# Kernel tuning notes

Hardware: AMD Instinct MI355X
Metric: run time of the kernel (lower is better)

The kernel has to match this reference:

```python
import jax, jax.numpy as jnp
import numpy as np

NPOINT = 1024   # npoint
K = 20          # num_samples[0]


def _fps(pts, npoint):
    """Iterative furthest point sampling. pts: [N,3] -> indices [npoint] (starts at idx 0)."""
    N = pts.shape[0]

    def step(carry, _):
        min_d, last = carry
        d = jnp.sum((pts - pts[last]) ** 2, axis=-1)          # [N] dist to last selected
        min_d = jnp.minimum(min_d, d)                          # running min-dist to selected set
        nxt = jnp.argmax(min_d).astype(jnp.int32)
        return (min_d, nxt), nxt

    init = (jnp.full((N,), 1e10, pts.dtype), jnp.int32(0))
    _, rest = jax.lax.scan(step, init, None, length=npoint - 1)
    return jnp.concatenate([jnp.zeros((1,), jnp.int32), rest])


def _pdist2(q, p):
    """Squared pairwise distances. q:[M,3], p:[N,3] -> [M,N], clamped to >=0 (matches pdist2squared)."""
    d = jnp.sum(q * q, -1)[:, None] + jnp.sum(p * p, -1)[None, :] - 2.0 * (q @ p.T)
    return jnp.maximum(d, 0.0)


def _knn(q, p, k):
    """k nearest neighbors of each q among p, dropping the closest (self), ascending order."""
    d = _pdist2(q, p)                       # [M,N]
    _, idx = jax.lax.top_k(-d, k + 1)       # ascending distance order
    return idx[:, 1:]                       # drop self, [M,k]


def setup_inputs() -> dict:
    key = jax.random.key(0)
    points = jax.random.normal(key, (4, 16384, 3), dtype=jnp.float32)
    return {"points": points}


def reference(points):
    B, N, _ = points.shape
    # --- FPS node sampling (Sample module) ---
    xyz_ind = jax.vmap(lambda p: _fps(p, NPOINT))(points)                  # [B, N1]
    xyz_query = jnp.take_along_axis(points, xyz_ind[:, :, None], axis=1)  # [B, N1, 3]

    # --- Gmid: neighbors of the N1 query points among all N points ---
    nbr_mid = jax.vmap(lambda q, p: _knn(q, p, K))(xyz_query, points)      # [B, N1, K]
    src_mid = jnp.take_along_axis(points, nbr_mid.reshape(B, -1, 1), axis=1).reshape(B, NPOINT, K, 3)
    d_mid = xyz_query[:, :, None, :] - src_mid                             # edata['d'] = pos[dst]-pos[src]

    # --- Gout: neighbors among the downsampled N1 points themselves ---
    nbr_out = jax.vmap(lambda q: _knn(q, q, K))(xyz_query)                 # [B, N1, K]
    src_out = jnp.take_along_axis(xyz_query, nbr_out.reshape(B, -1, 1), axis=1).reshape(B, NPOINT, K, 3)
    d_out = xyz_query[:, :, None, :] - src_out

    return xyz_ind, xyz_query, nbr_mid, d_mid, nbr_out, d_out
```

## Files before the change

kernel.cpp:

```cpp
#include <hip/hip_runtime.h>
#include <stdint.h>

#define BATCH   4
#define NPTS    16384
#define NPOINT  1024
#define KNN     20
#define KSEL    21

#define FPS_THREADS 512
#define PPT (NPTS / FPS_THREADS)

__global__ __launch_bounds__(FPS_THREADS)
void fps_kernel(const float* __restrict__ pts, float* __restrict__ out,
                int* __restrict__ ws_ind, float* __restrict__ ws_query) {
  const int b = blockIdx.x;
  const float* P = pts + (size_t)b * NPTS * 3;
  float* out_ind = out;
  float* out_q   = out + BATCH * NPOINT;
  const int t = threadIdx.x;

  float px[PPT], py[PPT], pz[PPT], md[PPT];
#pragma unroll
  for (int i = 0; i < PPT; ++i) {
    int idx = i * FPS_THREADS + t;
    px[i] = P[idx * 3 + 0];
    py[i] = P[idx * 3 + 1];
    pz[i] = P[idx * 3 + 2];
    md[i] = 1e10f;
  }

  __shared__ float s_val[FPS_THREADS / 64];
  __shared__ int   s_idx[FPS_THREADS / 64];

  if (t == 0) {
    out_ind[b * NPOINT] = 0.0f;
    ws_ind[b * NPOINT]  = 0;
    float ax = P[0], ay = P[1], az = P[2];
    out_q[(size_t)(b * NPOINT) * 3 + 0] = ax;
    out_q[(size_t)(b * NPOINT) * 3 + 1] = ay;
    out_q[(size_t)(b * NPOINT) * 3 + 2] = az;
    ws_query[(size_t)(b * NPOINT) * 3 + 0] = ax;
    ws_query[(size_t)(b * NPOINT) * 3 + 1] = ay;
    ws_query[(size_t)(b * NPOINT) * 3 + 2] = az;
  }
  float qx = P[0], qy = P[1], qz = P[2];

  for (int it = 1; it < NPOINT; ++it) {
    float best = -1.0f;
    int bi = 0;
#pragma unroll
    for (int i = 0; i < PPT; ++i) {
      float dx = __fsub_rn(px[i], qx);
      float dy = __fsub_rn(py[i], qy);
      float dz = __fsub_rn(pz[i], qz);
      float d  = __fadd_rn(__fadd_rn(__fmul_rn(dx, dx), __fmul_rn(dy, dy)),
                           __fmul_rn(dz, dz));
      float m = fminf(md[i], d);
      md[i] = m;
      if (m > best) { best = m; bi = i; }
    }
    int bidx = bi * FPS_THREADS + t;

#pragma unroll
    for (int off = 32; off >= 1; off >>= 1) {
      float ov = __shfl_down(best, off);
      int   oi = __shfl_down(bidx, off);
      if (ov > best || (ov == best && oi < bidx)) { best = ov; bidx = oi; }
    }

    __syncthreads();
    if ((t & 63) == 0) { s_val[t >> 6] = best; s_idx[t >> 6] = bidx; }
    __syncthreads();

    float bv = s_val[0];
    int   bx = s_idx[0];
#pragma unroll
    for (int w = 1; w < FPS_THREADS / 64; ++w) {
      float v = s_val[w];
      int   x = s_idx[w];
      if (v > bv || (v == bv && x < bx)) { bv = v; bx = x; }
    }

    qx = P[bx * 3 + 0];
    qy = P[bx * 3 + 1];
    qz = P[bx * 3 + 2];

    if (t == 0) {
      out_ind[b * NPOINT + it] = (float)bx;
      ws_ind[b * NPOINT + it]  = bx;
      size_t o = (size_t)(b * NPOINT + it) * 3;
      out_q[o + 0] = qx; out_q[o + 1] = qy; out_q[o + 2] = qz;
      ws_query[o + 0] = qx; ws_query[o + 1] = qy; ws_query[o + 2] = qz;
    }
  }
}

#define KNN_WAVES 4

__global__ __launch_bounds__(256)
void knn_kernel(const float* __restrict__ cand_base,
                const float* __restrict__ query_base,
                int ncand,
                float* __restrict__ out_nbr,
                float* __restrict__ out_d) {
#pragma clang fp contract(off)
  const int wid_in_blk = threadIdx.x >> 6;
  const int w    = blockIdx.x * KNN_WAVES + wid_in_blk;
  const int lane = threadIdx.x & 63;
  const int b    = w / NPOINT;
  const int qi   = w % NPOINT;

  const float* C = cand_base + (size_t)b * ncand * 3;
  const float* Q = query_base + ((size_t)b * NPOINT + qi) * 3;
  const float qx = Q[0], qy = Q[1], qz = Q[2];
  const float qq = (qx * qx + qy * qy) + qz * qz;

  unsigned long long best[KSEL];
#pragma unroll
  for (int j = 0; j < KSEL; ++j) best[j] = 0xFFFFFFFFFFFFFFFFull;

  for (int j = lane; j < ncand; j += 64) {
    float px = C[j * 3 + 0], py = C[j * 3 + 1], pz = C[j * 3 + 2];
    float pp  = (px * px + py * py) + pz * pz;
    float dot = __builtin_fmaf(qz, pz, __builtin_fmaf(qy, py, qx * px));
    float d = (qq + pp) - 2.0f * dot;
    d = fmaxf(d, 0.0f);
    unsigned long long key =
        ((unsigned long long)__float_as_uint(d) << 32) | (unsigned int)j;
    if (key < best[KSEL - 1]) {
      unsigned long long c = key;
#pragma unroll
      for (int s = 0; s < KSEL; ++s) {
        unsigned long long o = best[s];
        bool l = c < o;
        unsigned long long nb = l ? c : o;
        c = l ? o : c;
        best[s] = nb;
      }
    }
  }

  __shared__ unsigned long long s_list[KNN_WAVES][64 * KSEL];
  unsigned long long* L = s_list[wid_in_blk];
#pragma unroll
  for (int j = 0; j < KSEL; ++j) L[lane * KSEL + j] = best[j];
  __syncthreads();

  int hp = 0;
  int myK = -1, myIdx = 0;
  for (int r = 0; r < KSEL; ++r) {
    unsigned long long v = L[lane * KSEL + hp];
    int src = lane;
#pragma unroll
    for (int off = 32; off >= 1; off >>= 1) {
      unsigned long long ov = __shfl_down(v, off);
      int os = __shfl_down(src, off);
      if (ov < v) { v = ov; src = os; }
    }
    v   = __shfl(v, 0);
    src = __shfl(src, 0);
    if (lane == src) hp++;
    if (r >= 1 && lane == r - 1) {
      myIdx = (int)(unsigned int)(v & 0xFFFFFFFFull);
      myK = r - 1;
    }
  }

  if (myK >= 0) {
    size_t o = (size_t)(b * NPOINT + qi) * KNN + myK;
    out_nbr[o] = (float)myIdx;
    float sx = C[myIdx * 3 + 0], sy = C[myIdx * 3 + 1], sz = C[myIdx * 3 + 2];
    out_d[o * 3 + 0] = qx - sx;
    out_d[o * 3 + 1] = qy - sy;
    out_d[o * 3 + 2] = qz - sz;
  }
}

extern "C" void kernel_launch(void* const* d_in, const int* in_sizes, int n_in,
                              void* d_out, int out_size, void* d_ws,
                              size_t ws_size, hipStream_t stream) {
  (void)in_sizes; (void)n_in; (void)out_size; (void)ws_size;
  const float* pts = (const float*)d_in[0];
  float* out = (float*)d_out;

  int*   ws_ind   = (int*)d_ws;
  float* ws_query = (float*)((char*)d_ws + (size_t)BATCH * NPOINT * sizeof(int));

  float* out_nbr_mid = out + (size_t)BATCH * NPOINT * 4;
  float* out_d_mid   = out_nbr_mid + (size_t)BATCH * NPOINT * KNN;
  float* out_nbr_out = out_d_mid + (size_t)BATCH * NPOINT * KNN * 3;
  float* out_d_out   = out_nbr_out + (size_t)BATCH * NPOINT * KNN;

  hipLaunchKernelGGL(fps_kernel, dim3(BATCH), dim3(FPS_THREADS), 0, stream,
                     pts, out, ws_ind, ws_query);

  hipLaunchKernelGGL(knn_kernel, dim3(BATCH * NPOINT / KNN_WAVES), dim3(256),
                     0, stream, pts, ws_query, NPTS, out_nbr_mid, out_d_mid);

  hipLaunchKernelGGL(knn_kernel, dim3(BATCH * NPOINT / KNN_WAVES), dim3(256),
                     0, stream, ws_query, ws_query, NPOINT, out_nbr_out,
                     out_d_out);
}
```

Measured before the change: 2.868 ms.

## Split FPS across 16 cooperating blocks per batch with global atomic slot exchange

FPS now runs on 16 blocks per batch instead of one, each holding 4 points per thread, and reduces the per-iteration argmax across blocks through release/acquire atomic stores into an iteration-tagged slot array in the workspace. This spreads the serial sampling loop over many more CUs so each iteration does less per-thread work. In exchange every iteration pays a cross-block spin-wait through L2/global memory. The scheme also assumes all 64 blocks are co-resident, and it relies on the slot memory not already holding a matching iteration tag from an earlier run.

Measured after the change: 3.038 ms. 5.9% more time.

```diff
diff --git a/kernel.cpp b/kernel.cpp
--- a/kernel.cpp
+++ b/kernel.cpp
@@ -7,59 +7,71 @@
 #define KNN     20
 #define KSEL    21
 
-#define FPS_THREADS 512
-#define PPT (NPTS / FPS_THREADS)
-
-__global__ __launch_bounds__(FPS_THREADS)
+typedef unsigned long long u64;
+
+#define FPS_SUBS 16
+#define FPS_TPB  256
+#define FPS_GT   (FPS_SUBS * FPS_TPB)
+#define FPS_PPT  (NPTS / FPS_GT)
+
+#define REPEAT4(M) M(0) M(1) M(2) M(3)
+
+#define FPS_DECL(i) float px##i, py##i, pz##i, md##i;
+
+#define FPS_INIT(i) { \
+    int idx = (i) * FPS_GT + g; \
+    px##i = P[idx * 3 + 0]; \
+    py##i = P[idx * 3 + 1]; \
+    pz##i = P[idx * 3 + 2]; \
+    md##i = 1e10f; }
+
+#define FPS_STEP(i) { \
+    float dx = __fsub_rn(px##i, qx); \
+    float dy = __fsub_rn(py##i, qy); \
+    float dz = __fsub_rn(pz##i, qz); \
+    float d  = __fadd_rn(__fadd_rn(__fmul_rn(dx, dx), __fmul_rn(dy, dy)), \
+                         __fmul_rn(dz, dz)); \
+    float m = fminf(md##i, d); \
+    md##i = m; \
+    bool g2 = (m > best); \
+    best = g2 ? m : best; \
+    bi   = g2 ? (i) : bi; }
+
+__global__ __launch_bounds__(FPS_TPB)
 void fps_kernel(const float* __restrict__ pts, float* __restrict__ out,
-                int* __restrict__ ws_ind, float* __restrict__ ws_query) {
-  const int b = blockIdx.x;
+                int* __restrict__ ws_ind, float* __restrict__ ws_query,
+                u64* __restrict__ slots) {
+  const int blk = blockIdx.x;
+  const int b   = blk >> 4;
+  const int sub = blk & 15;
+  const int t   = threadIdx.x;
+  const int g   = sub * FPS_TPB + t;
   const float* P = pts + (size_t)b * NPTS * 3;
   float* out_ind = out;
   float* out_q   = out + BATCH * NPOINT;
-  const int t = threadIdx.x;
-
-  float px[PPT], py[PPT], pz[PPT], md[PPT];
-#pragma unroll
-  for (int i = 0; i < PPT; ++i) {
-    int idx = i * FPS_THREADS + t;
-    px[i] = P[idx * 3 + 0];
-    py[i] = P[idx * 3 + 1];
-    pz[i] = P[idx * 3 + 2];
-    md[i] = 1e10f;
-  }
-
-  __shared__ float s_val[FPS_THREADS / 64];
-  __shared__ int   s_idx[FPS_THREADS / 64];
-
-  if (t == 0) {
+
+  REPEAT4(FPS_DECL)
+  REPEAT4(FPS_INIT)
+
+  __shared__ float s_val[FPS_TPB / 64];
+  __shared__ int   s_idx[FPS_TPB / 64];
+  __shared__ int   s_widx;
+
+  if (sub == 0 && t == 0) {
     out_ind[b * NPOINT] = 0.0f;
     ws_ind[b * NPOINT]  = 0;
     float ax = P[0], ay = P[1], az = P[2];
-    out_q[(size_t)(b * NPOINT) * 3 + 0] = ax;
-    out_q[(size_t)(b * NPOINT) * 3 + 1] = ay;
-    out_q[(size_t)(b * NPOINT) * 3 + 2] = az;
-    ws_query[(size_t)(b * NPOINT) * 3 + 0] = ax;
-    ws_query[(size_t)(b * NPOINT) * 3 + 1] = ay;
-    ws_query[(size_t)(b * NPOINT) * 3 + 2] = az;
+    size_t o0 = (size_t)(b * NPOINT) * 3;
+    out_q[o0 + 0] = ax; out_q[o0 + 1] = ay; out_q[o0 + 2] = az;
+    ws_query[o0 + 0] = ax; ws_query[o0 + 1] = ay; ws_query[o0 + 2] = az;
   }
   float qx = P[0], qy = P[1], qz = P[2];
 
   for (int it = 1; it < NPOINT; ++it) {
     float best = -1.0f;
     int bi = 0;
-#pragma unroll
-    for (int i = 0; i < PPT; ++i) {
-      float dx = __fsub_rn(px[i], qx);
-      float dy = __fsub_rn(py[i], qy);
-      float dz = __fsub_rn(pz[i], qz);
-      float d  = __fadd_rn(__fadd_rn(__fmul_rn(dx, dx), __fmul_rn(dy, dy)),
-                           __fmul_rn(dz, dz));
-      float m = fminf(md[i], d);
-      md[i] = m;
-      if (m > best) { best = m; bi = i; }
-    }
-    int bidx = bi * FPS_THREADS + t;
+    REPEAT4(FPS_STEP)
+    int bidx = bi * FPS_GT + g;
 
 #pragma unroll
     for (int off = 32; off >= 1; off >>= 1) {
@@ -67,27 +79,52 @@
       int   oi = __shfl_down(bidx, off);
       if (ov > best || (ov == best && oi < bidx)) { best = ov; bidx = oi; }
     }
-
-    __syncthreads();
     if ((t & 63) == 0) { s_val[t >> 6] = best; s_idx[t >> 6] = bidx; }
     __syncthreads();
 
-    float bv = s_val[0];
-    int   bx = s_idx[0];
-#pragma unroll
-    for (int w = 1; w < FPS_THREADS / 64; ++w) {
-      float v = s_val[w];
-      int   x = s_idx[w];
-      if (v > bv || (v == bv && x < bx)) { bv = v; bx = x; }
-    }
-
-    qx = P[bx * 3 + 0];
-    qy = P[bx * 3 + 1];
-    qz = P[bx * 3 + 2];
-
-    if (t == 0) {
-      out_ind[b * NPOINT + it] = (float)bx;
-      ws_ind[b * NPOINT + it]  = bx;
+    if (t < 64) {
+      float bv = s_val[0];
+      int   bx = s_idx[0];
+#pragma unroll
+      for (int w = 1; w < FPS_TPB / 64; ++w) {
+        float v = s_val[w];
+        int   x = s_idx[w];
+        if (v > bv || (v == bv && x < bx)) { bv = v; bx = x; }
+      }
+      u64* row = slots + (size_t)it * (BATCH * FPS_SUBS) + b * FPS_SUBS;
+      if (t == 0) {
+        u64 pv = ((u64)__float_as_uint(bv) << 32) |
+                 (unsigned)(bx | (it << 20));
+        __hip_atomic_store(&row[sub], pv, __ATOMIC_RELEASE,
+                           __HIP_MEMORY_SCOPE_AGENT);
+      }
+      int j = t & 15;
+      u64 v;
+      do {
+        v = __hip_atomic_load(&row[j], __ATOMIC_ACQUIRE,
+                              __HIP_MEMORY_SCOPE_AGENT);
+      } while ((v >> 63) != 0 ||
+               (((unsigned)(v >> 20)) & 0x3FFu) != (unsigned)it);
+      float fv = __uint_as_float((unsigned)(v >> 32));
+      int   fi = (int)((unsigned)v & 0xFFFFFu);
+#pragma unroll
+      for (int off = 8; off >= 1; off >>= 1) {
+        float ofv = __shfl_down(fv, off);
+        int   ofi = __shfl_down(fi, off);
+        if (ofv > fv || (ofv == fv && ofi < fi)) { fv = ofv; fi = ofi; }
+      }
+      if (t == 0) s_widx = fi;
+    }
+    __syncthreads();
+    const int widx = s_widx;
+
+    qx = P[widx * 3 + 0];
+    qy = P[widx * 3 + 1];
+    qz = P[widx * 3 + 2];
+
+    if (sub == 0 && t == 0) {
+      out_ind[b * NPOINT + it] = (float)widx;
+      ws_ind[b * NPOINT + it]  = widx;
       size_t o = (size_t)(b * NPOINT + it) * 3;
       out_q[o + 0] = qx; out_q[o + 1] = qy; out_q[o + 2] = qz;
       ws_query[o + 0] = qx; ws_query[o + 1] = qy; ws_query[o + 2] = qz;
@@ -185,14 +222,15 @@
 
   int*   ws_ind   = (int*)d_ws;
   float* ws_query = (float*)((char*)d_ws + (size_t)BATCH * NPOINT * sizeof(int));
+  u64*   slots    = (u64*)((char*)d_ws + 64 * 1024);
 
   float* out_nbr_mid = out + (size_t)BATCH * NPOINT * 4;
   float* out_d_mid   = out_nbr_mid + (size_t)BATCH * NPOINT * KNN;
   float* out_nbr_out = out_d_mid + (size_t)BATCH * NPOINT * KNN * 3;
   float* out_d_out   = out_nbr_out + (size_t)BATCH * NPOINT * KNN;
 
-  hipLaunchKernelGGL(fps_kernel, dim3(BATCH), dim3(FPS_THREADS), 0, stream,
-                     pts, out, ws_ind, ws_query);
+  hipLaunchKernelGGL(fps_kernel, dim3(BATCH * FPS_SUBS), dim3(FPS_TPB), 0,
+                     stream, pts, out, ws_ind, ws_query, slots);
 
   hipLaunchKernelGGL(knn_kernel, dim3(BATCH * NPOINT / KNN_WAVES), dim3(256),
                      0, stream, pts, ws_query, NPTS, out_nbr_mid, out_d_mid);
```
